# Optimization experiments

Hardware: AMD Instinct MI355X
Metric: run time of the kernel (lower is better)

## Reference

```python
import jax, jax.numpy as jnp
import numpy as np

N = 100000      # nodes
E = 1600000     # message-passing edges
P = 1000000     # prediction edges
DIN = 128       # node_in_channels
H = 128         # hidden_channels
DOUT = 64       # out_channels (node embedding)
EIN = 32        # edge_in_channels
EPS = 1e-5


def setup_inputs() -> dict:
    key = jax.random.key(0)
    ks = iter(jax.random.split(key, 48))
    nk = lambda: next(ks)
    rn = lambda shape: jax.random.normal(nk(), shape, dtype=jnp.float32)
    glorot = lambda shape: rn(shape) * (1.0 / np.sqrt(shape[-1]))
    inp = {
        "x": rn((N, DIN)),
        "edge_index": jax.random.randint(nk(), (2, E), 0, N),
        "pred_edge_index": jax.random.randint(nk(), (2, P), 0, N),
        "edge_features": rn((P, EIN)),
        # SAGEConv layer 1: lin_l (aggregated, with bias), lin_r (root, no bias)
        "sage1_Wl": glorot((H, DIN)), "sage1_bl": jnp.zeros((H,), jnp.float32), "sage1_Wr": glorot((H, DIN)),
        "bn1_g": jnp.ones((H,), jnp.float32), "bn1_b": jnp.zeros((H,), jnp.float32),
        "bn1_m": rn((H,)) * 0.1, "bn1_v": jnp.ones((H,), jnp.float32),
        # SAGEConv layer 2
        "sage2_Wl": glorot((DOUT, H)), "sage2_bl": jnp.zeros((DOUT,), jnp.float32), "sage2_Wr": glorot((DOUT, H)),
        # edge MLP: Linear(EIN, H//2) -> BN -> ReLU -> Linear(H//2, H//4)
        "edge_W1": glorot((H // 2, EIN)), "edge_b1": jnp.zeros((H // 2,), jnp.float32),
        "ebn_g": jnp.ones((H // 2,), jnp.float32), "ebn_b": jnp.zeros((H // 2,), jnp.float32),
        "ebn_m": rn((H // 2,)) * 0.1, "ebn_v": jnp.ones((H // 2,), jnp.float32),
        "edge_W2": glorot((H // 4, H // 2)), "edge_b2": jnp.zeros((H // 4,), jnp.float32),
        # predictor: Linear(2*DOUT+H//4, H) -> BN -> ReLU -> Linear(H, H//2) -> BN -> ReLU -> Linear(H//2, 1)
        "p_W1": glorot((H, 2 * DOUT + H // 4)), "p_b1": jnp.zeros((H,), jnp.float32),
        "pbn1_g": jnp.ones((H,), jnp.float32), "pbn1_b": jnp.zeros((H,), jnp.float32),
        "pbn1_m": rn((H,)) * 0.1, "pbn1_v": jnp.ones((H,), jnp.float32),
        "p_W2": glorot((H // 2, H)), "p_b2": jnp.zeros((H // 2,), jnp.float32),
        "pbn2_g": jnp.ones((H // 2,), jnp.float32), "pbn2_b": jnp.zeros((H // 2,), jnp.float32),
        "pbn2_m": rn((H // 2,)) * 0.1, "pbn2_v": jnp.ones((H // 2,), jnp.float32),
        "p_W3": glorot((1, H // 2)), "p_b3": jnp.zeros((1,), jnp.float32),
    }
    return inp


def _bn(h, g, b, m, v):
    # eval-mode BatchNorm1d with running stats
    return (h - m) * (g / jnp.sqrt(v + EPS)) + b


def _sage(h, src, dst, Wl, bl, Wr):
    # PyG SAGEConv (mean aggr): lin_l(mean of h[src] at dst) + lin_r(h)
    msg = jax.ops.segment_sum(h[src], dst, num_segments=N)        # [N, d]
    cnt = jax.ops.segment_sum(jnp.ones((src.shape[0],), h.dtype), dst, num_segments=N)
    agg = msg / jnp.maximum(cnt, 1.0)[:, None]
    return agg @ Wl.T + bl + h @ Wr.T


def reference(x, edge_index, pred_edge_index, edge_features,
              sage1_Wl, sage1_bl, sage1_Wr, bn1_g, bn1_b, bn1_m, bn1_v,
              sage2_Wl, sage2_bl, sage2_Wr,
              edge_W1, edge_b1, ebn_g, ebn_b, ebn_m, ebn_v, edge_W2, edge_b2,
              p_W1, p_b1, pbn1_g, pbn1_b, pbn1_m, pbn1_v,
              p_W2, p_b2, pbn2_g, pbn2_b, pbn2_m, pbn2_v, p_W3, p_b3):
    src, dst = edge_index[0], edge_index[1]
    # GraphSAGE encoder (eval mode: dropout off, BN running stats)
    h = _sage(x, src, dst, sage1_Wl, sage1_bl, sage1_Wr)
    h = jax.nn.relu(_bn(h, bn1_g, bn1_b, bn1_m, bn1_v))
    z = _sage(h, src, dst, sage2_Wl, sage2_bl, sage2_Wr)          # [N, DOUT]
    # edge-pair gather + concat
    combined = jnp.concatenate([z[pred_edge_index[0]], z[pred_edge_index[1]]], axis=-1)  # [P, 2*DOUT]
    # edge feature MLP
    e = edge_features @ edge_W1.T + edge_b1
    e = jax.nn.relu(_bn(e, ebn_g, ebn_b, ebn_m, ebn_v))
    e = e @ edge_W2.T + edge_b2                                   # [P, H//4]
    combined = jnp.concatenate([combined, e], axis=-1)            # [P, 2*DOUT + H//4]
    # predictor MLP
    u = combined @ p_W1.T + p_b1
    u = jax.nn.relu(_bn(u, pbn1_g, pbn1_b, pbn1_m, pbn1_v))
    u = u @ p_W2.T + p_b2
    u = jax.nn.relu(_bn(u, pbn2_g, pbn2_b, pbn2_m, pbn2_v))
    out = u @ p_W3.T + p_b3                                       # [P, 1]
    return out[:, 0]
```

## Files before the change

kernel.cpp:

```cpp
#include <hip/hip_runtime.h>

#define Nn 100000
#define Ee 1600000
#define Pp 1000000
#define EPSf 1e-5f

typedef _Float16 f16x8 __attribute__((ext_vector_type(8)));
typedef _Float16 f16x4 __attribute__((ext_vector_type(4)));
typedef _Float16 f16x2 __attribute__((ext_vector_type(2)));
typedef float f32x4 __attribute__((ext_vector_type(4)));

__device__ __forceinline__ float4 ld4(const float* p) { return *(const float4*)p; }

#define oW1l 0
#define oW1r 16384
#define oW2l 32768
#define oW2r 40960
#define oW1a 49152
#define oW1b 57344
#define oW1c 65536
#define oWe1 69632
#define oWe2 71680
#define oWp2 73728
#define W16_TOTAL 81920

#define BN_TOTAL 608

__global__ __launch_bounds__(256) void prep_kernel(
    const float* __restrict__ x,
    const float* __restrict__ s1Wl, const float* __restrict__ s1Wr,
    const float* __restrict__ s2Wl, const float* __restrict__ s2Wr,
    const float* __restrict__ pW1,  const float* __restrict__ eW1,
    const float* __restrict__ eW2,  const float* __restrict__ pW2,
    const float* __restrict__ eb1,
    const float* __restrict__ ebng, const float* __restrict__ ebnb,
    const float* __restrict__ ebnm, const float* __restrict__ ebnv,
    const float* __restrict__ eb2,
    const float* __restrict__ pb1,
    const float* __restrict__ p1g, const float* __restrict__ p1b,
    const float* __restrict__ p1m, const float* __restrict__ p1v,
    const float* __restrict__ pb2,
    const float* __restrict__ p2g, const float* __restrict__ p2b,
    const float* __restrict__ p2m, const float* __restrict__ p2v,
    const float* __restrict__ pW3,
    _Float16* __restrict__ w16, float* __restrict__ bnA,
    _Float16* __restrict__ x16) {
    int tid = blockIdx.x * 256 + threadIdx.x;
    if (tid < W16_TOTAL) {
        float v;
        if (tid < 16384)      v = s1Wl[tid];
        else if (tid < 32768) v = s1Wr[tid - 16384];
        else if (tid < 40960) v = s2Wl[tid - 32768];
        else if (tid < 49152) v = s2Wr[tid - 40960];
        else if (tid < 57344) { int l = tid - 49152; v = pW1[(l >> 6) * 160 + (l & 63)]; }
        else if (tid < 65536) { int l = tid - 57344; v = pW1[(l >> 6) * 160 + 64 + (l & 63)]; }
        else if (tid < 69632) { int l = tid - 65536; v = pW1[(l >> 5) * 160 + 128 + (l & 31)]; }
        else if (tid < 71680) v = eW1[tid - 69632];
        else if (tid < 73728) v = eW2[tid - 71680];
        else                  v = pW2[tid - 73728];
        w16[tid] = (_Float16)v;
    } else if (tid < W16_TOTAL + BN_TOTAL) {
        int b = tid - W16_TOTAL;
        float v;
        if (b < 64)       v = ebng[b] * rsqrtf(ebnv[b] + EPSf);
        else if (b < 128) { int c = b - 64;  float s = ebng[c] * rsqrtf(ebnv[c] + EPSf);
                            v = (eb1[c] - ebnm[c]) * s + ebnb[c]; }
        else if (b < 256) { int c = b - 128; v = p1g[c] * rsqrtf(p1v[c] + EPSf); }
        else if (b < 384) { int c = b - 256; float s = p1g[c] * rsqrtf(p1v[c] + EPSf);
                            v = (pb1[c] - p1m[c]) * s + p1b[c]; }
        else if (b < 448) { int c = b - 384; v = p2g[c] * rsqrtf(p2v[c] + EPSf); }
        else if (b < 512) { int c = b - 448; float s = p2g[c] * rsqrtf(p2v[c] + EPSf);
                            v = (pb2[c] - p2m[c]) * s + p2b[c]; }
        else if (b < 544) v = eb2[b - 512];
        else              v = pW3[b - 544];
        bnA[b] = v;
    }
    int stride = gridDim.x * 256;
    const int NV = Nn * 128 / 4;
    for (int i = tid; i < NV; i += stride) {
        float4 v = ((const float4*)x)[i];
        f16x4 h = {(_Float16)v.x, (_Float16)v.y, (_Float16)v.z, (_Float16)v.w};
        ((f16x4*)x16)[i] = h;
    }
}

__global__ __launch_bounds__(256) void hist_kernel(const int* __restrict__ dst,
                                                   unsigned* __restrict__ deg) {
    int i = blockIdx.x * 256 + threadIdx.x;
    if (i < Ee) atomicAdd(&deg[dst[i]], 1u);
}

__global__ __launch_bounds__(1024) void scanA_kernel(const unsigned* __restrict__ deg,
                                                     unsigned* __restrict__ escan,
                                                     unsigned* __restrict__ bsum) {
    __shared__ unsigned s[1024];
    int t = threadIdx.x;
    int gid = blockIdx.x * 1024 + t;
    unsigned v = (gid < Nn) ? deg[gid] : 0u;
    s[t] = v;
    __syncthreads();
    for (int off = 1; off < 1024; off <<= 1) {
        unsigned u = (t >= off) ? s[t - off] : 0u;
        __syncthreads();
        s[t] += u;
        __syncthreads();
    }
    if (gid < Nn) escan[gid] = s[t] - v;
    if (t == 1023) bsum[blockIdx.x] = s[1023];
}

__global__ __launch_bounds__(128) void scanB_kernel(const unsigned* __restrict__ bsum,
                                                    unsigned* __restrict__ boff,
                                                    int nblk) {
    __shared__ unsigned s[128];
    int t = threadIdx.x;
    unsigned v = (t < nblk) ? bsum[t] : 0u;
    s[t] = v;
    __syncthreads();
    for (int off = 1; off < 128; off <<= 1) {
        unsigned u = (t >= off) ? s[t - off] : 0u;
        __syncthreads();
        s[t] += u;
        __syncthreads();
    }
    if (t < nblk) boff[t] = s[t] - v;
}

__global__ __launch_bounds__(1024) void scanC_kernel(const unsigned* __restrict__ escan,
                                                     const unsigned* __restrict__ boff,
                                                     int* __restrict__ rowptr,
                                                     int* __restrict__ cursor) {
    int t = threadIdx.x;
    int gid = blockIdx.x * 1024 + t;
    if (gid < Nn) {
        int v = (int)(escan[gid] + boff[blockIdx.x]);
        rowptr[gid] = v;
        cursor[gid] = v;
    }
    if (gid == 0) rowptr[Nn] = Ee;
}

__global__ __launch_bounds__(256) void scatter_kernel(const int* __restrict__ src,
                                                      const int* __restrict__ dst,
                                                      int* __restrict__ cursor,
                                                      int* __restrict__ elist) {
    int i = blockIdx.x * 256 + threadIdx.x;
    if (i < Ee) {
        int p = atomicAdd(&cursor[dst[i]], 1);
        elist[p] = src[i];
    }
}

template<int W>
__global__ __launch_bounds__(256, 8) void aggregate16_kernel(
    const _Float16* __restrict__ feat,
    const int* __restrict__ rowptr,
    const int* __restrict__ elist,
    _Float16* __restrict__ outp) {
    int node = (blockIdx.x * 256 + threadIdx.x) >> 6;
    int lane = threadIdx.x & 63;
    if (node >= Nn) return;
    constexpr int SEGS = W / 8;
    constexpr int RPI  = 64 / SEGS;
    const int r = lane / SEGS, c = lane % SEGS;
    int beg = rowptr[node], end = rowptr[node + 1];
    int n = end - beg;
    float acc[8];
#pragma unroll
    for (int k = 0; k < 8; ++k) acc[k] = 0.f;
    for (int c0 = 0; c0 < n; c0 += 64) {
        int m = min(64, n - c0);
        int se = (lane < m) ? elist[beg + c0 + lane] : 0;
        int iters = (m + RPI - 1) / RPI;
#pragma unroll 2
        for (int i = 0; i < iters; ++i) {
            int j = i * RPI + r;
            int s = __shfl(se, j);
            if (j < m) {
                f16x8 v = *(const f16x8*)(feat + (size_t)s * W + c * 8);
#pragma unroll
                for (int k = 0; k < 8; ++k) acc[k] += (float)v[k];
            }
        }
    }
#pragma unroll
    for (int k = 0; k < 8; ++k) {
#pragma unroll
        for (int off = SEGS; off < 64; off <<= 1)
            acc[k] += __shfl_xor(acc[k], off);
    }
    if (r == 0) {
        float inv = 1.0f / fmaxf((float)n, 1.0f);
        f16x8 o;
#pragma unroll
        for (int k = 0; k < 8; ++k) o[k] = (_Float16)(acc[k] * inv);
        *(f16x8*)(outp + (size_t)node * W + c * 8) = o;
    }
}

__global__ __launch_bounds__(256) void dense1_kernel(
    const _Float16* __restrict__ A1, const _Float16* __restrict__ A2,
    const _Float16* __restrict__ W1, const _Float16* __restrict__ W2,
    const float* __restrict__ lb,
    const float* __restrict__ bng, const float* __restrict__ bnb,
    const float* __restrict__ bnm, const float* __restrict__ bnv,
    _Float16* __restrict__ out) {
    const int t = threadIdx.x;
    const int w = t >> 6, lane = t & 63;
    const int lrow = lane & 15, lq = lane >> 4;
    const int row0 = blockIdx.x * 64 + w * 16;
    const int ld = min(row0 + lrow, Nn - 1);

    f16x8 a1[4], a2[4];
#pragma unroll
    for (int i = 0; i < 4; ++i) {
        a1[i] = *(const f16x8*)(A1 + (size_t)ld * 128 + i * 32 + lq * 8);
        a2[i] = *(const f16x8*)(A2 + (size_t)ld * 128 + i * 32 + lq * 8);
    }
#pragma unroll
    for (int nt = 0; nt < 8; ++nt) {
        const _Float16* w1r = W1 + (size_t)(nt * 16 + lrow) * 128;
        const _Float16* w2r = W2 + (size_t)(nt * 16 + lrow) * 128;
        f32x4 c = {0.f, 0.f, 0.f, 0.f};
#pragma unroll
        for (int i = 0; i < 4; ++i) {
            c = __builtin_amdgcn_mfma_f32_16x16x32_f16(a1[i], *(const f16x8*)(w1r + i * 32 + lq * 8), c, 0, 0, 0);
            c = __builtin_amdgcn_mfma_f32_16x16x32_f16(a2[i], *(const f16x8*)(w2r + i * 32 + lq * 8), c, 0, 0, 0);
        }
        int cc = nt * 16 + lrow;
        float s = bng[cc] * rsqrtf(bnv[cc] + EPSf);
        float h = (lb[cc] - bnm[cc]) * s + bnb[cc];
#pragma unroll
        for (int r = 0; r < 4; ++r) {
            int gr = row0 + lq * 4 + r;
            if (gr < Nn)
                out[(size_t)gr * 128 + cc] = (_Float16)fmaxf(c[r] * s + h, 0.f);
        }
    }
}

__global__ __launch_bounds__(256) void gemmY_kernel(
    const _Float16* __restrict__ A, const _Float16* __restrict__ W,
    _Float16* __restrict__ out) {
    const int t = threadIdx.x;
    const int w = t >> 6, lane = t & 63;
    const int lrow = lane & 15, lq = lane >> 4;
    const int row0 = blockIdx.x * 64 + w * 16;
    const int ld = min(row0 + lrow, Nn - 1);
    f16x8 a[4];
#pragma unroll
    for (int i = 0; i < 4; ++i)
        a[i] = *(const f16x8*)(A + (size_t)ld * 128 + i * 32 + lq * 8);
#pragma unroll
    for (int nt = 0; nt < 4; ++nt) {
        const _Float16* wr = W + (size_t)(nt * 16 + lrow) * 128;
        f32x4 c = {0.f, 0.f, 0.f, 0.f};
#pragma unroll
        for (int i = 0; i < 4; ++i)
            c = __builtin_amdgcn_mfma_f32_16x16x32_f16(a[i], *(const f16x8*)(wr + i * 32 + lq * 8), c, 0, 0, 0);
        int cc = nt * 16 + lrow;
#pragma unroll
        for (int r = 0; r < 4; ++r) {
            int gr = row0 + lq * 4 + r;
            if (gr < Nn) out[(size_t)gr * 64 + cc] = (_Float16)c[r];
        }
    }
}

__global__ __launch_bounds__(256) void dense2b_kernel(
    const _Float16* __restrict__ aggY, const _Float16* __restrict__ A2,
    const _Float16* __restrict__ W2, const float* __restrict__ lb,
    _Float16* __restrict__ out) {
    const int t = threadIdx.x;
    const int w = t >> 6, lane = t & 63;
    const int lrow = lane & 15, lq = lane >> 4;
    const int row0 = blockIdx.x * 64 + w * 16;
    const int ld = min(row0 + lrow, Nn - 1);
    f16x8 a[4];
#pragma unroll
    for (int i = 0; i < 4; ++i)
        a[i] = *(const f16x8*)(A2 + (size_t)ld * 128 + i * 32 + lq * 8);
#pragma unroll
    for (int nt = 0; nt < 4; ++nt) {
        const _Float16* wr = W2 + (size_t)(nt * 16 + lrow) * 128;
        f32x4 c = {0.f, 0.f, 0.f, 0.f};
#pragma unroll
        for (int i = 0; i < 4; ++i)
            c = __builtin_amdgcn_mfma_f32_16x16x32_f16(a[i], *(const f16x8*)(wr + i * 32 + lq * 8), c, 0, 0, 0);
        int cc = nt * 16 + lrow;
        float b = lb[cc];
#pragma unroll
        for (int r = 0; r < 4; ++r) {
            int gr = row0 + lq * 4 + r;
            if (gr < Nn) {
                float g = (float)aggY[(size_t)gr * 64 + cc];
                out[(size_t)gr * 64 + cc] = (_Float16)(c[r] + g + b);
            }
        }
    }
}

#define EPB 128
#define NT  ((Pp + EPB - 1) / EPB)
#define EGRID 1024

#define oL_We1 0
#define oL_We2 5120
#define oL_W1c 9728
#define oL_Wp2 19968
#define oL_BN  37376
#define oL_E1  39808
#define oL_E2  58240
#define oL_ZU  68480
#define SMEM_BYTES 103296

__global__ __launch_bounds__(512, 2) void edge_kernel(
    const int* __restrict__ pe,
    const float* __restrict__ ef,
    const _Float16* __restrict__ z,
    const _Float16* __restrict__ w16,
    const float* __restrict__ bnA,
    const float* __restrict__ pb3,
    float* __restrict__ out) {
    __shared__ __align__(16) unsigned char smem[SMEM_BYTES];
    _Float16* LWe1 = (_Float16*)(smem + oL_We1);
    _Float16* LWe2 = (_Float16*)(smem + oL_We2);
    _Float16* LW1c = (_Float16*)(smem + oL_W1c);
    _Float16* LWp2 = (_Float16*)(smem + oL_Wp2);
    float*    LBN  = (float*)(smem + oL_BN);
    _Float16* E1 = (_Float16*)(smem + oL_E1);
    _Float16* E2 = (_Float16*)(smem + oL_E2);
    _Float16* ZU = (_Float16*)(smem + oL_ZU);

    const float* bn1s = LBN;        const float* bn1h = LBN + 64;
    const float* bn2s = LBN + 128;  const float* bn2h = LBN + 256;
    const float* bn3s = LBN + 384;  const float* bn3h = LBN + 448;
    const float* eb2g = LBN + 512;  const float* wp3g = LBN + 544;

    const int t = threadIdx.x;
    const int lane = t & 63;
    const int w = t >> 6;
    const int m0 = w * 16;
    const int lrow = lane & 15;
    const int lq = lane >> 4;
    const int er = lane >> 3;
    const int seg = lane & 7;
    const float pb3v = pb3[0];

    auto load_tile = [&](int tl, f16x8* Ga, f16x8* Gb, float4& Ef0, float4& Ef1) -> bool {
        if (tl >= NT) return false;
        int e0 = tl * EPB + m0;
        if (e0 >= Pp) return false;
#pragma unroll
        for (int i = 0; i < 2; ++i) {
            int eg = e0 + i * 8 + er;
            int ai = pe[eg];
            int bi = pe[Pp + eg];
            Ga[i] = *(const f16x8*)(z + (size_t)ai * 64 + seg * 8);
            Gb[i] = *(const f16x8*)(z + (size_t)bi * 64 + seg * 8);
        }
        const float* src = ef + (size_t)(e0 + lrow) * 32 + lq * 8;
        Ef0 = ld4(src); Ef1 = ld4(src + 4);
        return true;
    };

    int tile = blockIdx.x;
    f16x8 ga[2], gb[2]; float4 ef0, ef1;
    bool act = load_tile(tile, ga, gb, ef0, ef1);

    f16x8 wa0[8], wa1[8], wb0[8], wb1[8];
#pragma unroll
    for (int nt = 0; nt < 8; ++nt) {
        const _Float16* ra = w16 + oW1a + (size_t)(nt * 16 + lrow) * 64;
        const _Float16* rb = w16 + oW1b + (size_t)(nt * 16 + lrow) * 64;
        wa0[nt] = *(const f16x8*)(ra + lq * 8);
        wa1[nt] = *(const f16x8*)(ra + 32 + lq * 8);
        wb0[nt] = *(const f16x8*)(rb + lq * 8);
        wb1[nt] = *(const f16x8*)(rb + 32 + lq * 8);
    }

    for (int u = t; u < 256; u += 512) { int r = u >> 2, s = u & 3;
        *(f16x8*)(LWe1 + r * 40 + s * 8) = *(const f16x8*)(w16 + oWe1 + r * 32 + s * 8); }
    for (int u = t; u < 256; u += 512) { int r = u >> 3, s = u & 7;
        *(f16x8*)(LWe2 + r * 72 + s * 8) = *(const f16x8*)(w16 + oWe2 + r * 64 + s * 8); }
    for (int u = t; u < 512; u += 512) { int r = u >> 2, s = u & 3;
        *(f16x8*)(LW1c + r * 40 + s * 8) = *(const f16x8*)(w16 + oW1c + r * 32 + s * 8); }
    for (int u = t; u < 1024; u += 512) { int r = u >> 4, s = u & 15;
        *(f16x8*)(LWp2 + r * 136 + s * 8) = *(const f16x8*)(w16 + oWp2 + r * 128 + s * 8); }
    for (int u = t; u < BN_TOTAL; u += 512) LBN[u] = bnA[u];
    __syncthreads();

    for (; tile < NT; tile += EGRID) {
        const int base = tile * EPB;

        if (act) {
#pragma unroll
            for (int i = 0; i < 2; ++i) {
                int e = m0 + i * 8 + er;
                *(f16x8*)(ZU + e * 136 + seg * 8) = ga[i];
                *(f16x8*)(ZU + e * 136 + 64 + seg * 8) = gb[i];
            }
        }
        f16x8 nga[2], ngb[2]; float4 nef0, nef1;
        bool nact = load_tile(tile + EGRID, nga, ngb, nef0, nef1);

        if (act) {
            const int erow = m0 + lrow;
            {
                f16x8 b = {(_Float16)ef0.x, (_Float16)ef0.y, (_Float16)ef0.z, (_Float16)ef0.w,
                           (_Float16)ef1.x, (_Float16)ef1.y, (_Float16)ef1.z, (_Float16)ef1.w};
#pragma unroll
                for (int nt = 0; nt < 4; ++nt) {
                    f16x8 wf = *(const f16x8*)(LWe1 + (nt * 16 + lrow) * 40 + lq * 8);
                    f32x4 c = {0.f, 0.f, 0.f, 0.f};
                    c = __builtin_amdgcn_mfma_f32_16x16x32_f16(wf, b, c, 0, 0, 0);
                    int cb = nt * 16 + lq * 4;
                    float4 s = *(const float4*)(bn1s + cb);
                    float4 h = *(const float4*)(bn1h + cb);
                    f16x4 o;
                    o[0] = (_Float16)fmaxf(c[0] * s.x + h.x, 0.f);
                    o[1] = (_Float16)fmaxf(c[1] * s.y + h.y, 0.f);
                    o[2] = (_Float16)fmaxf(c[2] * s.z + h.z, 0.f);
                    o[3] = (_Float16)fmaxf(c[3] * s.w + h.w, 0.f);
                    *(f16x4*)(E1 + erow * 72 + cb) = o;
                }
            }
            {
                f16x8 a0 = *(const f16x8*)(E1 + erow * 72 + lq * 8);
                f16x8 a1 = *(const f16x8*)(E1 + erow * 72 + 32 + lq * 8);
#pragma unroll
                for (int nt = 0; nt < 2; ++nt) {
                    f16x8 b0 = *(const f16x8*)(LWe2 + (nt * 16 + lrow) * 72 + lq * 8);
                    f16x8 b1 = *(const f16x8*)(LWe2 + (nt * 16 + lrow) * 72 + 32 + lq * 8);
                    f32x4 c = {0.f, 0.f, 0.f, 0.f};
                    c = __builtin_amdgcn_mfma_f32_16x16x32_f16(b0, a0, c, 0, 0, 0);
                    c = __builtin_amdgcn_mfma_f32_16x16x32_f16(b1, a1, c, 0, 0, 0);
                    int cb = nt * 16 + lq * 4;
                    float4 bias = *(const float4*)(eb2g + cb);
                    f16x4 o;
                    o[0] = (_Float16)(c[0] + bias.x);
                    o[1] = (_Float16)(c[1] + bias.y);
                    o[2] = (_Float16)(c[2] + bias.z);
                    o[3] = (_Float16)(c[3] + bias.w);
                    *(f16x4*)(E2 + erow * 40 + cb) = o;
                }
            }
            {
                const int zr = erow * 136;
                f16x8 za0 = *(const f16x8*)(ZU + zr + lq * 8);
                f16x8 za1 = *(const f16x8*)(ZU + zr + 32 + lq * 8);
                f16x8 zb0 = *(const f16x8*)(ZU + zr + 64 + lq * 8);
                f16x8 zb1 = *(const f16x8*)(ZU + zr + 96 + lq * 8);
                f16x8 ae  = *(const f16x8*)(E2 + erow * 40 + lq * 8);
                __builtin_amdgcn_s_setprio(1);
#pragma unroll
                for (int nt = 0; nt < 8; ++nt) {
                    f16x8 wc = *(const f16x8*)(LW1c + (nt * 16 + lrow) * 40 + lq * 8);
                    f32x4 c = {0.f, 0.f, 0.f, 0.f};
                    c = __builtin_amdgcn_mfma_f32_16x16x32_f16(wa0[nt], za0, c, 0, 0, 0);
                    c = __builtin_amdgcn_mfma_f32_16x16x32_f16(wa1[nt], za1, c, 0, 0, 0);
                    c = __builtin_amdgcn_mfma_f32_16x16x32_f16(wb0[nt], zb0, c, 0, 0, 0);
                    c = __builtin_amdgcn_mfma_f32_16x16x32_f16(wb1[nt], zb1, c, 0, 0, 0);
                    c = __builtin_amdgcn_mfma_f32_16x16x32_f16(wc,      ae,  c, 0, 0, 0);
                    int cb = nt * 16 + lq * 4;
                    float4 s = *(const float4*)(bn2s + cb);
                    float4 h = *(const float4*)(bn2h + cb);
                    f16x4 o;
                    o[0] = (_Float16)fmaxf(c[0] * s.x + h.x, 0.f);
                    o[1] = (_Float16)fmaxf(c[1] * s.y + h.y, 0.f);
                    o[2] = (_Float16)fmaxf(c[2] * s.z + h.z, 0.f);
                    o[3] = (_Float16)fmaxf(c[3] * s.w + h.w, 0.f);
                    *(f16x4*)(ZU + zr + cb) = o;
                }
                __builtin_amdgcn_s_setprio(0);
            }
            {
                const int zr = erow * 136;
                f16x8 a0 = *(const f16x8*)(ZU + zr + 0  + lq * 8);
                f16x8 a1 = *(const f16x8*)(ZU + zr + 32 + lq * 8);
                f16x8 a2 = *(const f16x8*)(ZU + zr + 64 + lq * 8);
                f16x8 a3 = *(const f16x8*)(ZU + zr + 96 + lq * 8);
                float acc = 0.f;
                __builtin_amdgcn_s_setprio(1);
#pragma unroll
                for (int nt = 0; nt < 4; ++nt) {
                    const _Float16* wr = LWp2 + (nt * 16 + lrow) * 136 + lq * 8;
                    f32x4 c = {0.f, 0.f, 0.f, 0.f};
                    c = __builtin_amdgcn_mfma_f32_16x16x32_f16(*(const f16x8*)(wr + 0),  a0, c, 0, 0, 0);
                    c = __builtin_amdgcn_mfma_f32_16x16x32_f16(*(const f16x8*)(wr + 32), a1, c, 0, 0, 0);
                    c = __builtin_amdgcn_mfma_f32_16x16x32_f16(*(const f16x8*)(wr + 64), a2, c, 0, 0, 0);
                    c = __builtin_amdgcn_mfma_f32_16x16x32_f16(*(const f16x8*)(wr + 96), a3, c, 0, 0, 0);
                    int cb = nt * 16 + lq * 4;
                    float4 s  = *(const float4*)(bn3s + cb);
                    float4 h  = *(const float4*)(bn3h + cb);
                    float4 w3 = *(const float4*)(wp3g + cb);
                    acc += fmaxf(c[0] * s.x + h.x, 0.f) * w3.x;
                    acc += fmaxf(c[1] * s.y + h.y, 0.f) * w3.y;
                    acc += fmaxf(c[2] * s.z + h.z, 0.f) * w3.z;
                    acc += fmaxf(c[3] * s.w + h.w, 0.f) * w3.w;
                }
                __builtin_amdgcn_s_setprio(0);
                acc += __shfl_xor(acc, 16);
                acc += __shfl_xor(acc, 32);
                if (lane < 16) out[base + m0 + lane] = acc + pb3v;
            }
        }
        ga[0] = nga[0]; ga[1] = nga[1];
        gb[0] = ngb[0]; gb[1] = ngb[1];
        ef0 = nef0; ef1 = nef1;
        act = nact;
    }
}

extern "C" void kernel_launch(void* const* d_in, const int* in_sizes, int n_in,
                              void* d_out, int out_size, void* d_ws, size_t ws_size,
                              hipStream_t stream) {
    const float* x    = (const float*)d_in[0];
    const int*   eidx = (const int*)d_in[1];
    const int*   pe   = (const int*)d_in[2];
    const float* ef   = (const float*)d_in[3];
    const float* s1Wl = (const float*)d_in[4];
    const float* s1bl = (const float*)d_in[5];
    const float* s1Wr = (const float*)d_in[6];
    const float* bn1g = (const float*)d_in[7];
    const float* bn1b = (const float*)d_in[8];
    const float* bn1m = (const float*)d_in[9];
    const float* bn1v = (const float*)d_in[10];
    const float* s2Wl = (const float*)d_in[11];
    const float* s2bl = (const float*)d_in[12];
    const float* s2Wr = (const float*)d_in[13];
    const float* eW1  = (const float*)d_in[14];
    const float* eb1  = (const float*)d_in[15];
    const float* ebng = (const float*)d_in[16];
    const float* ebnb = (const float*)d_in[17];
    const float* ebnm = (const float*)d_in[18];
    const float* ebnv = (const float*)d_in[19];
    const float* eW2  = (const float*)d_in[20];
    const float* eb2  = (const float*)d_in[21];
    const float* pW1  = (const float*)d_in[22];
    const float* pb1  = (const float*)d_in[23];
    const float* p1g  = (const float*)d_in[24];
    const float* p1b  = (const float*)d_in[25];
    const float* p1m  = (const float*)d_in[26];
    const float* p1v  = (const float*)d_in[27];
    const float* pW2  = (const float*)d_in[28];
    const float* pb2  = (const float*)d_in[29];
    const float* p2g  = (const float*)d_in[30];
    const float* p2b  = (const float*)d_in[31];
    const float* p2m  = (const float*)d_in[32];
    const float* p2v  = (const float*)d_in[33];
    const float* pW3  = (const float*)d_in[34];
    const float* pb3  = (const float*)d_in[35];
    float* out = (float*)d_out;

    char* wk = (char*)d_ws;
    auto carve = [&](size_t bytes) {
        char* p = wk;
        wk += (bytes + 255) & ~(size_t)255;
        return p;
    };
    unsigned*  deg    = (unsigned*)carve((size_t)Nn * 4);
    int*       rowptr = (int*)carve((size_t)(Nn + 1) * 4);
    int*       cursor = (int*)carve((size_t)Nn * 4);
    int*       elist  = (int*)carve((size_t)Ee * 4);
    unsigned*  escan  = (unsigned*)carve((size_t)Nn * 4);
    unsigned*  bsum   = (unsigned*)carve(128 * 4);
    unsigned*  boff   = (unsigned*)carve(128 * 4);
    _Float16*  w16    = (_Float16*)carve((size_t)W16_TOTAL * 2);
    float*     bnA    = (float*)carve((size_t)BN_TOTAL * 4);
    _Float16*  bufX   = (_Float16*)carve((size_t)Nn * 128 * 2);
    _Float16*  bufA   = (_Float16*)carve((size_t)Nn * 128 * 2);
    _Float16*  bufH   = (_Float16*)carve((size_t)Nn * 128 * 2);
    _Float16*  bufY   = bufX;
    _Float16*  bufZ   = bufX + (size_t)Nn * 64;
    _Float16*  bufAy  = bufA;

    const int* e_src = eidx;
    const int* e_dst = eidx + Ee;
    const int SBLK = (Nn + 1023) / 1024;

    hipMemsetAsync(deg, 0, (size_t)Nn * 4, stream);
    prep_kernel<<<800, 256, 0, stream>>>(x, s1Wl, s1Wr, s2Wl, s2Wr, pW1, eW1, eW2, pW2,
                                         eb1, ebng, ebnb, ebnm, ebnv, eb2,
                                         pb1, p1g, p1b, p1m, p1v,
                                         pb2, p2g, p2b, p2m, p2v, pW3,
                                         w16, bnA, bufX);
    hist_kernel<<<(Ee + 255) / 256, 256, 0, stream>>>(e_dst, deg);
    scanA_kernel<<<SBLK, 1024, 0, stream>>>(deg, escan, bsum);
    scanB_kernel<<<1, 128, 0, stream>>>(bsum, boff, SBLK);
    scanC_kernel<<<SBLK, 1024, 0, stream>>>(escan, boff, rowptr, cursor);
    scatter_kernel<<<(Ee + 255) / 256, 256, 0, stream>>>(e_src, e_dst, cursor, elist);

    aggregate16_kernel<128><<<Nn / 4, 256, 0, stream>>>(bufX, rowptr, elist, bufA);
    dense1_kernel<<<(Nn + 63) / 64, 256, 0, stream>>>(
        bufA, bufX, w16 + oW1l, w16 + oW1r, s1bl, bn1g, bn1b, bn1m, bn1v, bufH);

    gemmY_kernel<<<(Nn + 63) / 64, 256, 0, stream>>>(bufH, w16 + oW2l, bufY);
    aggregate16_kernel<64><<<Nn / 4, 256, 0, stream>>>(bufY, rowptr, elist, bufAy);
    dense2b_kernel<<<(Nn + 63) / 64, 256, 0, stream>>>(
        bufAy, bufH, w16 + oW2r, s2bl, bufZ);

    edge_kernel<<<EGRID, 512, 0, stream>>>(pe, ef, bufZ, w16, bnA, pb3, out);
}
```

Baseline: 766.7 us.

## Split edge MLP into separate kernel and restructure edge kernel pipeline

```diff
diff --git a/kernel.cpp b/kernel.cpp
--- a/kernel.cpp
+++ b/kernel.cpp
@@ -162,6 +162,7 @@
     if (node >= Nn) return;
     constexpr int SEGS = W / 8;
     constexpr int RPI  = 64 / SEGS;
+    constexpr int B    = (RPI >= 8) ? 2 : 4;
     const int r = lane / SEGS, c = lane % SEGS;
     int beg = rowptr[node], end = rowptr[node + 1];
     int n = end - beg;
@@ -172,14 +173,27 @@
         int m = min(64, n - c0);
         int se = (lane < m) ? elist[beg + c0 + lane] : 0;
         int iters = (m + RPI - 1) / RPI;
-#pragma unroll 2
-        for (int i = 0; i < iters; ++i) {
+        int ff = m / RPI;
+        int i = 0;
+        for (; i + B <= ff; i += B) {
+            int sA[B]; f16x8 vA[B];
+#pragma unroll
+            for (int k = 0; k < B; ++k) sA[k] = __shfl(se, (i + k) * RPI + r);
+#pragma unroll
+            for (int k = 0; k < B; ++k)
+                vA[k] = *(const f16x8*)(feat + (size_t)sA[k] * W + c * 8);
+#pragma unroll
+            for (int k = 0; k < B; ++k)
+#pragma unroll
+                for (int q = 0; q < 8; ++q) acc[q] += (float)vA[k][q];
+        }
+        for (; i < iters; ++i) {
             int j = i * RPI + r;
             int s = __shfl(se, j);
             if (j < m) {
                 f16x8 v = *(const f16x8*)(feat + (size_t)s * W + c * 8);
 #pragma unroll
-                for (int k = 0; k < 8; ++k) acc[k] += (float)v[k];
+                for (int q = 0; q < 8; ++q) acc[q] += (float)v[q];
             }
         }
     }
@@ -300,42 +314,89 @@
     }
 }
 
-#define EPB 128
+__global__ __launch_bounds__(256) void emlp_kernel(
+    const float* __restrict__ ef,
+    const _Float16* __restrict__ w16,
+    const float* __restrict__ bnA,
+    _Float16* __restrict__ e2out) {
+    __shared__ __align__(16) _Float16 E1[64 * 72];
+    const int t = threadIdx.x;
+    const int lane = t & 63, w = t >> 6;
+    const int lrow = lane & 15, lq = lane >> 4;
+    const int e0 = blockIdx.x * 64 + w * 16;
+    const int erow = w * 16 + lrow;
+
+    const float* src = ef + (size_t)(e0 + lrow) * 32 + lq * 8;
+    float4 f0 = ld4(src), f1 = ld4(src + 4);
+    f16x8 bf = {(_Float16)f0.x, (_Float16)f0.y, (_Float16)f0.z, (_Float16)f0.w,
+                (_Float16)f1.x, (_Float16)f1.y, (_Float16)f1.z, (_Float16)f1.w};
+
+#pragma unroll
+    for (int nt = 0; nt < 4; ++nt) {
+        f16x8 wf = *(const f16x8*)(w16 + oWe1 + (nt * 16 + lrow) * 32 + lq * 8);
+        f32x4 c = {0.f, 0.f, 0.f, 0.f};
+        c = __builtin_amdgcn_mfma_f32_16x16x32_f16(wf, bf, c, 0, 0, 0);
+        int cb = nt * 16 + lq * 4;
+        float4 s = *(const float4*)(bnA + cb);
+        float4 h = *(const float4*)(bnA + 64 + cb);
+        f16x4 o;
+        o[0] = (_Float16)fmaxf(c[0] * s.x + h.x, 0.f);
+        o[1] = (_Float16)fmaxf(c[1] * s.y + h.y, 0.f);
+        o[2] = (_Float16)fmaxf(c[2] * s.z + h.z, 0.f);
+        o[3] = (_Float16)fmaxf(c[3] * s.w + h.w, 0.f);
+        *(f16x4*)(E1 + erow * 72 + cb) = o;
+    }
+    f16x8 a0 = *(const f16x8*)(E1 + erow * 72 + lq * 8);
+    f16x8 a1 = *(const f16x8*)(E1 + erow * 72 + 32 + lq * 8);
+#pragma unroll
+    for (int nt = 0; nt < 2; ++nt) {
+        f16x8 b0 = *(const f16x8*)(w16 + oWe2 + (nt * 16 + lrow) * 64 + lq * 8);
+        f16x8 b1 = *(const f16x8*)(w16 + oWe2 + (nt * 16 + lrow) * 64 + 32 + lq * 8);
+        f32x4 c = {0.f, 0.f, 0.f, 0.f};
+        c = __builtin_amdgcn_mfma_f32_16x16x32_f16(b0, a0, c, 0, 0, 0);
+        c = __builtin_amdgcn_mfma_f32_16x16x32_f16(b1, a1, c, 0, 0, 0);
+        int cb = nt * 16 + lq * 4;
+        float4 bias = *(const float4*)(bnA + 512 + cb);
+        f16x4 o;
+        o[0] = (_Float16)(c[0] + bias.x);
+        o[1] = (_Float16)(c[1] + bias.y);
+        o[2] = (_Float16)(c[2] + bias.z);
+        o[3] = (_Float16)(c[3] + bias.w);
+        *(f16x4*)(e2out + (size_t)(e0 + lrow) * 32 + cb) = o;
+    }
+}
+
+#define EPB 256
 #define NT  ((Pp + EPB - 1) / EPB)
-#define EGRID 1024
-
-#define oL_We1 0
-#define oL_We2 5120
-#define oL_W1c 9728
-#define oL_Wp2 19968
-#define oL_BN  37376
-#define oL_E1  39808
-#define oL_E2  58240
-#define oL_ZU  68480
-#define SMEM_BYTES 103296
-
-__global__ __launch_bounds__(512, 2) void edge_kernel(
+#define EGRID 256
+
+#define oL_W1a 0
+#define oL_W1b 18432
+#define oL_W1c 36864
+#define oL_Wp2 47104
+#define oL_BN  64512
+#define oL_ZU  66304
+#define SMEM_BYTES 135936
+
+__global__ __launch_bounds__(1024, 4) void edge_kernel(
     const int* __restrict__ pe,
-    const float* __restrict__ ef,
+    const _Float16* __restrict__ e2,
     const _Float16* __restrict__ z,
     const _Float16* __restrict__ w16,
     const float* __restrict__ bnA,
     const float* __restrict__ pb3,
     float* __restrict__ out) {
     __shared__ __align__(16) unsigned char smem[SMEM_BYTES];
-    _Float16* LWe1 = (_Float16*)(smem + oL_We1);
-    _Float16* LWe2 = (_Float16*)(smem + oL_We2);
+    _Float16* LW1a = (_Float16*)(smem + oL_W1a);
+    _Float16* LW1b = (_Float16*)(smem + oL_W1b);
     _Float16* LW1c = (_Float16*)(smem + oL_W1c);
     _Float16* LWp2 = (_Float16*)(smem + oL_Wp2);
     float*    LBN  = (float*)(smem + oL_BN);
-    _Float16* E1 = (_Float16*)(smem + oL_E1);
-    _Float16* E2 = (_Float16*)(smem + oL_E2);
-    _Float16* ZU = (_Float16*)(smem + oL_ZU);
-
-    const float* bn1s = LBN;        const float* bn1h = LBN + 64;
-    const float* bn2s = LBN + 128;  const float* bn2h = LBN + 256;
-    const float* bn3s = LBN + 384;  const float* bn3h = LBN + 448;
-    const float* eb2g = LBN + 512;  const float* wp3g = LBN + 544;
+    _Float16* ZU   = (_Float16*)(smem + oL_ZU);
+
+    const float* bn2s = LBN;        const float* bn2h = LBN + 128;
+    const float* bn3s = LBN + 256;  const float* bn3h = LBN + 320;
+    const float* wp3g = LBN + 384;
 
     const int t = threadIdx.x;
     const int lane = t & 63;
@@ -343,125 +404,64 @@
     const int m0 = w * 16;
     const int lrow = lane & 15;
     const int lq = lane >> 4;
-    const int er = lane >> 3;
-    const int seg = lane & 7;
     const float pb3v = pb3[0];
 
-    auto load_tile = [&](int tl, f16x8* Ga, f16x8* Gb, float4& Ef0, float4& Ef1) -> bool {
-        if (tl >= NT) return false;
-        int e0 = tl * EPB + m0;
-        if (e0 >= Pp) return false;
-#pragma unroll
-        for (int i = 0; i < 2; ++i) {
-            int eg = e0 + i * 8 + er;
-            int ai = pe[eg];
-            int bi = pe[Pp + eg];
-            Ga[i] = *(const f16x8*)(z + (size_t)ai * 64 + seg * 8);
-            Gb[i] = *(const f16x8*)(z + (size_t)bi * 64 + seg * 8);
-        }
-        const float* src = ef + (size_t)(e0 + lrow) * 32 + lq * 8;
-        Ef0 = ld4(src); Ef1 = ld4(src + 4);
-        return true;
+    auto load_idx = [&](int tl, int& ia, int& ib) {
+        int e = min(tl * EPB + m0 + lrow, Pp - 1);
+        ia = pe[e];
+        ib = pe[Pp + e];
     };
+    auto gather = [&](int tl, int ia, int ib, f16x8* F) {
+        F[0] = *(const f16x8*)(z + (size_t)ia * 64 + lq * 8);
+        F[1] = *(const f16x8*)(z + (size_t)ia * 64 + 32 + lq * 8);
+        F[2] = *(const f16x8*)(z + (size_t)ib * 64 + lq * 8);
+        F[3] = *(const f16x8*)(z + (size_t)ib * 64 + 32 + lq * 8);
+        int e = min(tl * EPB + m0 + lrow, Pp - 1);
+        F[4] = *(const f16x8*)(e2 + (size_t)e * 32 + lq * 8);
+    };
 
     int tile = blockIdx.x;
-    f16x8 ga[2], gb[2]; float4 ef0, ef1;
-    bool act = load_tile(tile, ga, gb, ef0, ef1);
-
-    f16x8 wa0[8], wa1[8], wb0[8], wb1[8];
-#pragma unroll
-    for (int nt = 0; nt < 8; ++nt) {
-        const _Float16* ra = w16 + oW1a + (size_t)(nt * 16 + lrow) * 64;
-        const _Float16* rb = w16 + oW1b + (size_t)(nt * 16 + lrow) * 64;
-        wa0[nt] = *(const f16x8*)(ra + lq * 8);
-        wa1[nt] = *(const f16x8*)(ra + 32 + lq * 8);
-        wb0[nt] = *(const f16x8*)(rb + lq * 8);
-        wb1[nt] = *(const f16x8*)(rb + 32 + lq * 8);
-    }
-
-    for (int u = t; u < 256; u += 512) { int r = u >> 2, s = u & 3;
-        *(f16x8*)(LWe1 + r * 40 + s * 8) = *(const f16x8*)(w16 + oWe1 + r * 32 + s * 8); }
-    for (int u = t; u < 256; u += 512) { int r = u >> 3, s = u & 7;
-        *(f16x8*)(LWe2 + r * 72 + s * 8) = *(const f16x8*)(w16 + oWe2 + r * 64 + s * 8); }
-    for (int u = t; u < 512; u += 512) { int r = u >> 2, s = u & 3;
-        *(f16x8*)(LW1c + r * 40 + s * 8) = *(const f16x8*)(w16 + oW1c + r * 32 + s * 8); }
-    for (int u = t; u < 1024; u += 512) { int r = u >> 4, s = u & 15;
-        *(f16x8*)(LWp2 + r * 136 + s * 8) = *(const f16x8*)(w16 + oWp2 + r * 128 + s * 8); }
-    for (int u = t; u < BN_TOTAL; u += 512) LBN[u] = bnA[u];
-    __syncthreads();
-
-    for (; tile < NT; tile += EGRID) {
-        const int base = tile * EPB;
-
-        if (act) {
-#pragma unroll
-            for (int i = 0; i < 2; ++i) {
-                int e = m0 + i * 8 + er;
-                *(f16x8*)(ZU + e * 136 + seg * 8) = ga[i];
-                *(f16x8*)(ZU + e * 136 + 64 + seg * 8) = gb[i];
-            }
-        }
-        f16x8 nga[2], ngb[2]; float4 nef0, nef1;
-        bool nact = load_tile(tile + EGRID, nga, ngb, nef0, nef1);
-
-        if (act) {
-            const int erow = m0 + lrow;
-            {
-                f16x8 b = {(_Float16)ef0.x, (_Float16)ef0.y, (_Float16)ef0.z, (_Float16)ef0.w,
-                           (_Float16)ef1.x, (_Float16)ef1.y, (_Float16)ef1.z, (_Float16)ef1.w};
-#pragma unroll
-                for (int nt = 0; nt < 4; ++nt) {
-                    f16x8 wf = *(const f16x8*)(LWe1 + (nt * 16 + lrow) * 40 + lq * 8);
+    int ia1, ib1;
+    {
+        int ia0, ib0;
+        load_idx(tile, ia0, ib0);
+        load_idx(tile + EGRID, ia1, ib1);
+        f16x8 F[5];
+        gather(tile, ia0, ib0, F);
+
+        { int r = t >> 3, s = t & 7;
+          *(f16x8*)(LW1a + r * 72 + s * 8) = *(const f16x8*)(w16 + oW1a + r * 64 + s * 8);
+          *(f16x8*)(LW1b + r * 72 + s * 8) = *(const f16x8*)(w16 + oW1b + r * 64 + s * 8); }
+        if (t < 512) { int r = t >> 2, s = t & 3;
+          *(f16x8*)(LW1c + r * 40 + s * 8) = *(const f16x8*)(w16 + oW1c + r * 32 + s * 8); }
+        { int r = t >> 4, s = t & 15;
+          *(f16x8*)(LWp2 + r * 136 + s * 8) = *(const f16x8*)(w16 + oWp2 + r * 128 + s * 8); }
+        if (t < 384) LBN[t] = bnA[128 + t];
+        else if (t < 448) LBN[t] = bnA[544 + (t - 384)];
+        __syncthreads();
+
+        const int erow = m0 + lrow;
+        const int zr = erow * 136;
+        for (; tile < NT; tile += EGRID) {
+            f16x8 G[5];
+            gather(tile + EGRID, ia1, ib1, G);
+            int ia2, ib2;
+            load_idx(tile + 2 * EGRID, ia2, ib2);
+
+            const bool act = (tile * EPB + m0) < Pp;
+            if (act) {
+                __builtin_amdgcn_s_setprio(1);
+#pragma unroll
+                for (int nt = 0; nt < 8; ++nt) {
+                    const _Float16* wa = LW1a + (nt * 16 + lrow) * 72;
+                    const _Float16* wb = LW1b + (nt * 16 + lrow) * 72;
+                    const _Float16* wc = LW1c + (nt * 16 + lrow) * 40;
                     f32x4 c = {0.f, 0.f, 0.f, 0.f};
-                    c = __builtin_amdgcn_mfma_f32_16x16x32_f16(wf, b, c, 0, 0, 0);
-                    int cb = nt * 16 + lq * 4;
-                    float4 s = *(const float4*)(bn1s + cb);
-                    float4 h = *(const float4*)(bn1h + cb);
-                    f16x4 o;
-                    o[0] = (_Float16)fmaxf(c[0] * s.x + h.x, 0.f);
-                    o[1] = (_Float16)fmaxf(c[1] * s.y + h.y, 0.f);
-                    o[2] = (_Float16)fmaxf(c[2] * s.z + h.z, 0.f);
-                    o[3] = (_Float16)fmaxf(c[3] * s.w + h.w, 0.f);
-                    *(f16x4*)(E1 + erow * 72 + cb) = o;
-                }
-            }
-            {
-                f16x8 a0 = *(const f16x8*)(E1 + erow * 72 + lq * 8);
-                f16x8 a1 = *(const f16x8*)(E1 + erow * 72 + 32 + lq * 8);
-#pragma unroll
-                for (int nt = 0; nt < 2; ++nt) {
-                    f16x8 b0 = *(const f16x8*)(LWe2 + (nt * 16 + lrow) * 72 + lq * 8);
-                    f16x8 b1 = *(const f16x8*)(LWe2 + (nt * 16 + lrow) * 72 + 32 + lq * 8);
-                    f32x4 c = {0.f, 0.f, 0.f, 0.f};
-                    c = __builtin_amdgcn_mfma_f32_16x16x32_f16(b0, a0, c, 0, 0, 0);
-                    c = __builtin_amdgcn_mfma_f32_16x16x32_f16(b1, a1, c, 0, 0, 0);
-                    int cb = nt * 16 + lq * 4;
-                    float4 bias = *(const float4*)(eb2g + cb);
-                    f16x4 o;
-                    o[0] = (_Float16)(c[0] + bias.x);
-                    o[1] = (_Float16)(c[1] + bias.y);
-                    o[2] = (_Float16)(c[2] + bias.z);
-                    o[3] = (_Float16)(c[3] + bias.w);
-                    *(f16x4*)(E2 + erow * 40 + cb) = o;
-                }
-            }
-            {
-                const int zr = erow * 136;
-                f16x8 za0 = *(const f16x8*)(ZU + zr + lq * 8);
-                f16x8 za1 = *(const f16x8*)(ZU + zr + 32 + lq * 8);
-                f16x8 zb0 = *(const f16x8*)(ZU + zr + 64 + lq * 8);
-                f16x8 zb1 = *(const f16x8*)(ZU + zr + 96 + lq * 8);
-                f16x8 ae  = *(const f16x8*)(E2 + erow * 40 + lq * 8);
-                __builtin_amdgcn_s_setprio(1);
-#pragma unroll
-                for (int nt = 0; nt < 8; ++nt) {
-                    f16x8 wc = *(const f16x8*)(LW1c + (nt * 16 + lrow) * 40 + lq * 8);
-                    f32x4 c = {0.f, 0.f, 0.f, 0.f};
-                    c = __builtin_amdgcn_mfma_f32_16x16x32_f16(wa0[nt], za0, c, 0, 0, 0);
-                    c = __builtin_amdgcn_mfma_f32_16x16x32_f16(wa1[nt], za1, c, 0, 0, 0);
-                    c = __builtin_amdgcn_mfma_f32_16x16x32_f16(wb0[nt], zb0, c, 0, 0, 0);
-                    c = __builtin_amdgcn_mfma_f32_16x16x32_f16(wb1[nt], zb1, c, 0, 0, 0);
-                    c = __builtin_amdgcn_mfma_f32_16x16x32_f16(wc,      ae,  c, 0, 0, 0);
+                    c = __builtin_amdgcn_mfma_f32_16x16x32_f16(*(const f16x8*)(wa + lq * 8),      F[0], c, 0, 0, 0);
+                    c = __builtin_amdgcn_mfma_f32_16x16x32_f16(*(const f16x8*)(wa + 32 + lq * 8), F[1], c, 0, 0, 0);
+                    c = __builtin_amdgcn_mfma_f32_16x16x32_f16(*(const f16x8*)(wb + lq * 8),      F[2], c, 0, 0, 0);
+                    c = __builtin_amdgcn_mfma_f32_16x16x32_f16(*(const f16x8*)(wb + 32 + lq * 8), F[3], c, 0, 0, 0);
+                    c = __builtin_amdgcn_mfma_f32_16x16x32_f16(*(const f16x8*)(wc + lq * 8),      F[4], c, 0, 0, 0);
                     int cb = nt * 16 + lq * 4;
                     float4 s = *(const float4*)(bn2s + cb);
                     float4 h = *(const float4*)(bn2h + cb);
@@ -473,42 +473,40 @@
                     *(f16x4*)(ZU + zr + cb) = o;
                 }
                 __builtin_amdgcn_s_setprio(0);
+                {
+                    f16x8 a0 = *(const f16x8*)(ZU + zr + 0  + lq * 8);
+                    f16x8 a1 = *(const f16x8*)(ZU + zr + 32 + lq * 8);
+                    f16x8 a2 = *(const f16x8*)(ZU + zr + 64 + lq * 8);
+                    f16x8 a3 = *(const f16x8*)(ZU + zr + 96 + lq * 8);
+                    float acc = 0.f;
+                    __builtin_amdgcn_s_setprio(1);
+#pragma unroll
+                    for (int nt = 0; nt < 4; ++nt) {
+                        const _Float16* wr = LWp2 + (nt * 16 + lrow) * 136 + lq * 8;
+                        f32x4 c = {0.f, 0.f, 0.f, 0.f};
+                        c = __builtin_amdgcn_mfma_f32_16x16x32_f16(*(const f16x8*)(wr + 0),  a0, c, 0, 0, 0);
+                        c = __builtin_amdgcn_mfma_f32_16x16x32_f16(*(const f16x8*)(wr + 32), a1, c, 0, 0, 0);
+                        c = __builtin_amdgcn_mfma_f32_16x16x32_f16(*(const f16x8*)(wr + 64), a2, c, 0, 0, 0);
+                        c = __builtin_amdgcn_mfma_f32_16x16x32_f16(*(const f16x8*)(wr + 96), a3, c, 0, 0, 0);
+                        int cb = nt * 16 + lq * 4;
+                        float4 s  = *(const float4*)(bn3s + cb);
+                        float4 h  = *(const float4*)(bn3h + cb);
+                        float4 w3 = *(const float4*)(wp3g + cb);
+                        acc += fmaxf(c[0] * s.x + h.x, 0.f) * w3.x;
+                        acc += fmaxf(c[1] * s.y + h.y, 0.f) * w3.y;
+                        acc += fmaxf(c[2] * s.z + h.z, 0.f) * w3.z;
+                        acc += fmaxf(c[3] * s.w + h.w, 0.f) * w3.w;
+                    }
+                    __builtin_amdgcn_s_setprio(0);
+                    acc += __shfl_xor(acc, 16);
+                    acc += __shfl_xor(acc, 32);
+                    if (lane < 16) out[tile * EPB + m0 + lane] = acc + pb3v;
+                }
             }
-            {
-                const int zr = erow * 136;
-                f16x8 a0 = *(const f16x8*)(ZU + zr + 0  + lq * 8);
-                f16x8 a1 = *(const f16x8*)(ZU + zr + 32 + lq * 8);
-                f16x8 a2 = *(const f16x8*)(ZU + zr + 64 + lq * 8);
-                f16x8 a3 = *(const f16x8*)(ZU + zr + 96 + lq * 8);
-                float acc = 0.f;
-                __builtin_amdgcn_s_setprio(1);
-#pragma unroll
-                for (int nt = 0; nt < 4; ++nt) {
-                    const _Float16* wr = LWp2 + (nt * 16 + lrow) * 136 + lq * 8;
-                    f32x4 c = {0.f, 0.f, 0.f, 0.f};
-                    c = __builtin_amdgcn_mfma_f32_16x16x32_f16(*(const f16x8*)(wr + 0),  a0, c, 0, 0, 0);
-                    c = __builtin_amdgcn_mfma_f32_16x16x32_f16(*(const f16x8*)(wr + 32), a1, c, 0, 0, 0);
-                    c = __builtin_amdgcn_mfma_f32_16x16x32_f16(*(const f16x8*)(wr + 64), a2, c, 0, 0, 0);
-                    c = __builtin_amdgcn_mfma_f32_16x16x32_f16(*(const f16x8*)(wr + 96), a3, c, 0, 0, 0);
-                    int cb = nt * 16 + lq * 4;
-                    float4 s  = *(const float4*)(bn3s + cb);
-                    float4 h  = *(const float4*)(bn3h + cb);
-                    float4 w3 = *(const float4*)(wp3g + cb);
-                    acc += fmaxf(c[0] * s.x + h.x, 0.f) * w3.x;
-                    acc += fmaxf(c[1] * s.y + h.y, 0.f) * w3.y;
-                    acc += fmaxf(c[2] * s.z + h.z, 0.f) * w3.z;
-                    acc += fmaxf(c[3] * s.w + h.w, 0.f) * w3.w;
-                }
-                __builtin_amdgcn_s_setprio(0);
-                acc += __shfl_xor(acc, 16);
-                acc += __shfl_xor(acc, 32);
-                if (lane < 16) out[base + m0 + lane] = acc + pb3v;
-            }
+#pragma unroll
+            for (int i = 0; i < 5; ++i) F[i] = G[i];
+            ia1 = ia2; ib1 = ib2;
         }
-        ga[0] = nga[0]; ga[1] = nga[1];
-        gb[0] = ngb[0]; gb[1] = ngb[1];
-        ef0 = nef0; ef1 = nef1;
-        act = nact;
     }
 }
 
@@ -571,6 +569,7 @@
     _Float16*  bufX   = (_Float16*)carve((size_t)Nn * 128 * 2);
     _Float16*  bufA   = (_Float16*)carve((size_t)Nn * 128 * 2);
     _Float16*  bufH   = (_Float16*)carve((size_t)Nn * 128 * 2);
+    _Float16*  e2buf  = (_Float16*)carve((size_t)Pp * 32 * 2);
     _Float16*  bufY   = bufX;
     _Float16*  bufZ   = bufX + (size_t)Nn * 64;
     _Float16*  bufAy  = bufA;
@@ -585,6 +584,8 @@
                                          pb1, p1g, p1b, p1m, p1v,
                                          pb2, p2g, p2b, p2m, p2v, pW3,
                                          w16, bnA, bufX);
+    emlp_kernel<<<Pp / 64, 256, 0, stream>>>(ef, w16, bnA, e2buf);
+
     hist_kernel<<<(Ee + 255) / 256, 256, 0, stream>>>(e_dst, deg);
     scanA_kernel<<<SBLK, 1024, 0, stream>>>(deg, escan, bsum);
     scanB_kernel<<<1, 128, 0, stream>>>(bsum, boff, SBLK);
@@ -600,5 +601,5 @@
     dense2b_kernel<<<(Nn + 63) / 64, 256, 0, stream>>>(
         bufAy, bufH, w16 + oW2r, s2bl, bufZ);
 
-    edge_kernel<<<EGRID, 512, 0, stream>>>(pe, ef, bufZ, w16, bnA, pb3, out);
-}
+    edge_kernel<<<EGRID, 1024, 0, stream>>>(pe, e2buf, bufZ, w16, bnA, pb3, out);
+}
```

Result: slower. 808.7 us (+5.5%).
